# Performance work log

Hardware: AMD Instinct MI355X
Metric: run time of the kernel (lower is better)

## Reference

```python
import jax, jax.numpy as jnp
import numpy as np

TEMPERATURE = 5.656854249492381  # sqrt(d_k)=sqrt(32)


def setup_inputs() -> dict:
    key = jax.random.key(0)
    k1, k2, k3, k4 = jax.random.split(key, 4)
    B, L, H, DK, DV = 4, 1024, 8, 32, 32
    q = jax.random.normal(k1, (B, L, H * DK), dtype=jnp.float32)
    k = jax.random.normal(k2, (B, L, H * DK), dtype=jnp.float32)
    v = jax.random.normal(k3, (B, L, H * DV), dtype=jnp.float32)
    a_k = jax.random.normal(k4, (L, L, DK), dtype=jnp.float32)
    return {"q": q, "k": k, "v": v, "a_k": a_k, "d_k": DK, "d_v": DV, "n_head": H}


def reference(q, k, v, a_k, d_k, d_v, n_head):
    B, Lq, _ = q.shape
    Lv = v.shape[1]
    # [B, H, L, d]
    rq = q.reshape(B, Lq, n_head, d_k).transpose(0, 2, 1, 3)
    rk = k.reshape(B, Lq, n_head, d_k).transpose(0, 2, 1, 3)
    rv = v.reshape(B, Lv, n_head, d_v).transpose(0, 2, 1, 3)
    # attn[b,h,i,j] = sum_d rq[b,h,j,d] * rk[b,h,i,d] * a_k[i,j,d]
    # (dim 2 indexes k positions, dim 3 indexes q positions, per the torch broadcast)
    attn = jnp.einsum('bhjd,bhid,ijd->bhij', rq, rk, a_k) / TEMPERATURE
    attn = jax.nn.softmax(attn, axis=-1)
    # dropout is identity in eval mode
    out = jnp.einsum('bhij,bhjd->bhid', attn, rv)
    return out, attn
```

## Files before the change

kernel.cpp:

```cpp
#include <hip/hip_runtime.h>
#include <cstddef>

#define B_  4
#define L_  1024
#define H_  8
#define DK_ 32
#define DV_ 32
#define BH_ 32
#define HD_ 256

#define INV_T 0.17677669529663687f

__global__ __launch_bounds__(256) void transpose_q(
    const float* __restrict__ q, float* __restrict__ qT)
{
    const int bh  = blockIdx.x >> 2;
    const int jt  = blockIdx.x & 3;
    const int b   = bh >> 3, h = bh & 7;
    const int tid = threadIdx.x;

    __shared__ float t_s[256][33];

    const float* qb = q + (size_t)b * L_ * HD_ + h * DK_;
    #pragma unroll
    for (int rep = 0; rep < 8; ++rep) {
        const int f = rep * 1024 + tid * 4;
        const int j = f >> 5, d = f & 31;
        float4 val = *reinterpret_cast<const float4*>(qb + (size_t)(jt * 256 + j) * HD_ + d);
        t_s[j][d + 0] = val.x; t_s[j][d + 1] = val.y;
        t_s[j][d + 2] = val.z; t_s[j][d + 3] = val.w;
    }
    __syncthreads();
    float* qo = qT + (size_t)bh * (DK_ * L_);
    const int j = jt * 256 + tid;
    #pragma unroll
    for (int d4 = 0; d4 < 8; ++d4) {
        float4 w = make_float4(t_s[tid][d4 * 4 + 0], t_s[tid][d4 * 4 + 1],
                               t_s[tid][d4 * 4 + 2], t_s[tid][d4 * 4 + 3]);
        *reinterpret_cast<float4*>(qo + (size_t)d4 * (L_ * 4) + (size_t)j * 4) = w;
    }
}

__global__ __launch_bounds__(256) void score_kernel(
    const float* __restrict__ qT,
    const float* __restrict__ k,
    const float* __restrict__ a_k,
    float* __restrict__ attn_u,
    float* __restrict__ sums)
{
    const int bidx  = blockIdx.x;
    const int jhalf = bidx & 1;
    const int half  = (bidx >> 1) & 1;
    const int ig    = bidx >> 2;
    const int i0    = ig * 2;
    const int bh0   = half * 16;
    const int tid   = threadIdx.x;
    const int w     = __builtin_amdgcn_readfirstlane(tid >> 6);
    const int lane  = tid & 63;

    __shared__ float a_s[2][64][36];

    float rs[4][2] = {{0.f}};

    for (int jt = jhalf * 8; jt < jhalf * 8 + 8; ++jt) {
        const int j0 = jt * 64;
        __syncthreads();
        #pragma unroll
        for (int rep = 0; rep < 4; ++rep) {
            const int f  = rep * 1024 + tid * 4;
            const int ii = f >> 11, jj = (f >> 5) & 63, d = f & 31;
            float4 val = *reinterpret_cast<const float4*>(
                a_k + (size_t)(i0 + ii) * (L_ * DK_) + (size_t)(j0 + jj) * DK_ + d);
            *reinterpret_cast<float4*>(&a_s[ii][jj][d]) = val;
        }
        __syncthreads();

        float s[4][2];
        #pragma unroll
        for (int bhl = 0; bhl < 4; ++bhl)
            #pragma unroll
            for (int ii = 0; ii < 2; ++ii) s[bhl][ii] = 0.f;

        #pragma unroll 2
        for (int d4 = 0; d4 < 8; ++d4) {
            float4 av[2];
            #pragma unroll
            for (int ii = 0; ii < 2; ++ii)
                av[ii] = *reinterpret_cast<const float4*>(&a_s[ii][lane][d4 * 4]);
            #pragma unroll
            for (int bhl = 0; bhl < 4; ++bhl) {
                const int bh = bh0 + w * 4 + bhl;
                const int b  = bh >> 3, h = bh & 7;
                const float4 q4 = *reinterpret_cast<const float4*>(
                    qT + (size_t)bh * (DK_ * L_) + (size_t)d4 * (L_ * 4) + (size_t)(j0 + lane) * 4);
                const float* kp = k + (size_t)b * L_ * HD_ + (size_t)i0 * HD_ + h * DK_ + d4 * 4;
                #pragma unroll
                for (int ii = 0; ii < 2; ++ii) {
                    float4 kv = *reinterpret_cast<const float4*>(kp + ii * HD_);
                    s[bhl][ii] = fmaf(kv.x * av[ii].x, q4.x, s[bhl][ii]);
                    s[bhl][ii] = fmaf(kv.y * av[ii].y, q4.y, s[bhl][ii]);
                    s[bhl][ii] = fmaf(kv.z * av[ii].z, q4.z, s[bhl][ii]);
                    s[bhl][ii] = fmaf(kv.w * av[ii].w, q4.w, s[bhl][ii]);
                }
            }
        }

        #pragma unroll
        for (int bhl = 0; bhl < 4; ++bhl) {
            const int bh = bh0 + w * 4 + bhl;
            #pragma unroll
            for (int ii = 0; ii < 2; ++ii) {
                const float u = __expf(s[bhl][ii] * INV_T);
                rs[bhl][ii] += u;
                attn_u[((size_t)bh * L_ + (i0 + ii)) * L_ + j0 + lane] = u;
            }
        }
    }

    #pragma unroll
    for (int bhl = 0; bhl < 4; ++bhl) {
        #pragma unroll
        for (int ii = 0; ii < 2; ++ii) {
            float vsum = rs[bhl][ii];
            #pragma unroll
            for (int off = 32; off > 0; off >>= 1) vsum += __shfl_xor(vsum, off);
            if (lane == 0)
                sums[((size_t)jhalf * BH_ + bh0 + w * 4 + bhl) * L_ + i0 + ii] = vsum;
        }
    }
}

__global__ __launch_bounds__(256) void pv_kernel(
    const float* __restrict__ v,
    const float* __restrict__ sums,
    float* __restrict__ attn,
    float* __restrict__ out)
{
    const int bh  = blockIdx.x >> 6;
    const int ic  = blockIdx.x & 63;
    const int i0  = ic * 16;
    const int b   = bh >> 3, h = bh & 7;
    const int tid = threadIdx.x;
    const int r   = tid >> 4;
    const int t16 = tid & 15;

    __shared__ float v_s[64][36];
    __shared__ float u_s[16][68];

    const float inv = 1.0f / (sums[(size_t)bh * L_ + i0 + r] +
                              sums[(size_t)(BH_ + bh) * L_ + i0 + r]);
    float* arow = attn + ((size_t)bh * L_ + i0 + r) * L_;

    float a0 = 0.f, a1 = 0.f;

    for (int jt = 0; jt < 16; ++jt) {
        const int j0 = jt * 64;
        __syncthreads();
        {
            const int jj = tid >> 2, dv = (tid & 3) * 8;
            const float* vp = v + (size_t)b * L_ * HD_ + (size_t)(j0 + jj) * HD_ + h * DV_ + dv;
            float4 v0 = *reinterpret_cast<const float4*>(vp);
            float4 v1 = *reinterpret_cast<const float4*>(vp + 4);
            *reinterpret_cast<float4*>(&v_s[jj][dv])     = v0;
            *reinterpret_cast<float4*>(&v_s[jj][dv + 4]) = v1;
        }
        {
            float4 u0 = *reinterpret_cast<const float4*>(arow + j0 + t16 * 4);
            u0.x *= inv; u0.y *= inv; u0.z *= inv; u0.w *= inv;
            *reinterpret_cast<float4*>(&u_s[r][t16 * 4]) = u0;
            *reinterpret_cast<float4*>(arow + j0 + t16 * 4) = u0;
        }
        __syncthreads();
        #pragma unroll
        for (int jj4 = 0; jj4 < 16; ++jj4) {
            const float4 u4 = *reinterpret_cast<const float4*>(&u_s[r][jj4 * 4]);
            const float2 vv0 = *reinterpret_cast<const float2*>(&v_s[jj4 * 4 + 0][t16 * 2]);
            const float2 vv1 = *reinterpret_cast<const float2*>(&v_s[jj4 * 4 + 1][t16 * 2]);
            const float2 vv2 = *reinterpret_cast<const float2*>(&v_s[jj4 * 4 + 2][t16 * 2]);
            const float2 vv3 = *reinterpret_cast<const float2*>(&v_s[jj4 * 4 + 3][t16 * 2]);
            a0 = fmaf(u4.x, vv0.x, a0); a1 = fmaf(u4.x, vv0.y, a1);
            a0 = fmaf(u4.y, vv1.x, a0); a1 = fmaf(u4.y, vv1.y, a1);
            a0 = fmaf(u4.z, vv2.x, a0); a1 = fmaf(u4.z, vv2.y, a1);
            a0 = fmaf(u4.w, vv3.x, a0); a1 = fmaf(u4.w, vv3.y, a1);
        }
    }
    *reinterpret_cast<float2*>(out + ((size_t)bh * L_ + i0 + r) * DV_ + t16 * 2)
        = make_float2(a0, a1);
}

extern "C" void kernel_launch(void* const* d_in, const int* in_sizes, int n_in,
                              void* d_out, int out_size, void* d_ws, size_t ws_size,
                              hipStream_t stream) {
    const float* q   = (const float*)d_in[0];
    const float* k   = (const float*)d_in[1];
    const float* v   = (const float*)d_in[2];
    const float* a_k = (const float*)d_in[3];

    float* out  = (float*)d_out;
    float* attn = out + (size_t)BH_ * L_ * DV_;

    float* ws   = (float*)d_ws;
    float* sums = ws;
    float* qT   = ws + 2 * BH_ * L_;

    transpose_q<<<dim3(128),   dim3(256), 0, stream>>>(q, qT);
    score_kernel<<<dim3(2048), dim3(256), 0, stream>>>(qT, k, a_k, attn, sums);
    pv_kernel<<<dim3(2048),    dim3(256), 0, stream>>>(v, sums, attn, out);
}
```

Before: 408.4 us.

## Double-buffer score and PV tiles with direct global-to-LDS loads and XOR swizzle

```diff
diff --git a/kernel.cpp b/kernel.cpp
--- a/kernel.cpp
+++ b/kernel.cpp
@@ -1,5 +1,6 @@
 #include <hip/hip_runtime.h>
 #include <cstddef>
+#include <cstdint>
 
 #define B_  4
 #define L_  1024
@@ -10,6 +11,13 @@
 #define HD_ 256
 
 #define INV_T 0.17677669529663687f
+
+__device__ __forceinline__ void gload_lds16(const void* g, void* l) {
+    __builtin_amdgcn_global_load_lds(
+        (const __attribute__((address_space(1))) void*)g,
+        (__attribute__((address_space(3))) void*)l,
+        16, 0, 0);
+}
 
 __global__ __launch_bounds__(256) void transpose_q(
     const float* __restrict__ q, float* __restrict__ qT)
@@ -58,22 +66,40 @@
     const int w     = __builtin_amdgcn_readfirstlane(tid >> 6);
     const int lane  = tid & 63;
 
-    __shared__ float a_s[2][64][36];
+    __shared__ __align__(16) float a_s[2][2][64][32];
+
+    int s_ii[4], s_jj[4], s_c[4];
+    #pragma unroll
+    for (int r2 = 0; r2 < 4; ++r2) {
+        const int off = r2 * 4096 + tid * 16;
+        s_ii[r2] = off >> 13;
+        s_jj[r2] = (off >> 7) & 63;
+        s_c[r2]  = ((off >> 4) & 7) ^ (s_jj[r2] & 7);
+    }
+
+    auto STAGE = [&](int buf, int j0s) {
+        #pragma unroll
+        for (int r2 = 0; r2 < 4; ++r2) {
+            const float* src = a_k + (size_t)(i0 + s_ii[r2]) * (L_ * DK_)
+                             + (size_t)(j0s + s_jj[r2]) * DK_ + s_c[r2] * 4;
+            float* dst = (float*)((char*)(&a_s[buf][0][0][0]) + r2 * 4096 + w * 1024);
+            gload_lds16(src, dst);
+        }
+    };
 
     float rs[4][2] = {{0.f}};
-
-    for (int jt = jhalf * 8; jt < jhalf * 8 + 8; ++jt) {
-        const int j0 = jt * 64;
-        __syncthreads();
-        #pragma unroll
-        for (int rep = 0; rep < 4; ++rep) {
-            const int f  = rep * 1024 + tid * 4;
-            const int ii = f >> 11, jj = (f >> 5) & 63, d = f & 31;
-            float4 val = *reinterpret_cast<const float4*>(
-                a_k + (size_t)(i0 + ii) * (L_ * DK_) + (size_t)(j0 + jj) * DK_ + d);
-            *reinterpret_cast<float4*>(&a_s[ii][jj][d]) = val;
-        }
-        __syncthreads();
+    const int jt0 = jhalf * 8, jtE = jt0 + 8;
+    int cur = 0;
+
+    STAGE(0, jt0 * 64);
+    asm volatile("s_waitcnt vmcnt(0)" ::: "memory");
+    __builtin_amdgcn_s_barrier();
+
+    for (int jt = jt0; jt < jtE; ++jt) {
+        const int j0   = jt * 64;
+        const bool more = (jt != jtE - 1);
+
+        if (more) STAGE(cur ^ 1, j0 + 64);
 
         float s[4][2];
         #pragma unroll
@@ -86,7 +112,9 @@
             float4 av[2];
             #pragma unroll
             for (int ii = 0; ii < 2; ++ii)
-                av[ii] = *reinterpret_cast<const float4*>(&a_s[ii][lane][d4 * 4]);
+                av[ii] = *reinterpret_cast<const float4*>(
+                    (const char*)(&a_s[cur][ii][0][0]) + lane * 128
+                    + ((d4 ^ (lane & 7)) << 4));
             #pragma unroll
             for (int bhl = 0; bhl < 4; ++bhl) {
                 const int bh = bh0 + w * 4 + bhl;
@@ -115,6 +143,12 @@
                 attn_u[((size_t)bh * L_ + (i0 + ii)) * L_ + j0 + lane] = u;
             }
         }
+
+        if (more) {
+            asm volatile("s_waitcnt vmcnt(0)" ::: "memory");
+            __builtin_amdgcn_s_barrier();
+            cur ^= 1;
+        }
     }
 
     #pragma unroll
@@ -141,51 +175,73 @@
     const int i0  = ic * 16;
     const int b   = bh >> 3, h = bh & 7;
     const int tid = threadIdx.x;
+    const int w   = __builtin_amdgcn_readfirstlane(tid >> 6);
     const int r   = tid >> 4;
     const int t16 = tid & 15;
 
-    __shared__ float v_s[64][36];
-    __shared__ float u_s[16][68];
+    __shared__ __align__(16) float v_s[2][64][32];
+    __shared__ __align__(16) float u_s[2][16][64];
 
     const float inv = 1.0f / (sums[(size_t)bh * L_ + i0 + r] +
                               sums[(size_t)(BH_ + bh) * L_ + i0 + r]);
     float* arow = attn + ((size_t)bh * L_ + i0 + r) * L_;
 
+    const int u_c = t16 ^ (r & 3);
+    const float* u_src0 = arow + u_c * 4;
+    const float* vbase = v + (size_t)b * L_ * HD_ + h * DV_;
+    const int v_jj0 = tid >> 3, v_dc = tid & 7;
+
+    auto STAGE = [&](int buf, int j0s) {
+        gload_lds16(u_src0 + j0s, (float*)((char*)(&u_s[buf][0][0]) + w * 1024));
+        #pragma unroll
+        for (int s2 = 0; s2 < 2; ++s2)
+            gload_lds16(vbase + (size_t)(j0s + s2 * 32 + v_jj0) * HD_ + v_dc * 4,
+                        (float*)((char*)(&v_s[buf][0][0]) + s2 * 4096 + w * 1024));
+    };
+
     float a0 = 0.f, a1 = 0.f;
+    int cur = 0;
+
+    STAGE(0, 0);
+    asm volatile("s_waitcnt vmcnt(0)" ::: "memory");
+    __builtin_amdgcn_s_barrier();
 
     for (int jt = 0; jt < 16; ++jt) {
-        const int j0 = jt * 64;
-        __syncthreads();
+        const int j0   = jt * 64;
+        const bool more = (jt != 15);
+
+        if (more) STAGE(cur ^ 1, j0 + 64);
+
         {
-            const int jj = tid >> 2, dv = (tid & 3) * 8;
-            const float* vp = v + (size_t)b * L_ * HD_ + (size_t)(j0 + jj) * HD_ + h * DV_ + dv;
-            float4 v0 = *reinterpret_cast<const float4*>(vp);
-            float4 v1 = *reinterpret_cast<const float4*>(vp + 4);
-            *reinterpret_cast<float4*>(&v_s[jj][dv])     = v0;
-            *reinterpret_cast<float4*>(&v_s[jj][dv + 4]) = v1;
-        }
-        {
-            float4 u0 = *reinterpret_cast<const float4*>(arow + j0 + t16 * 4);
-            u0.x *= inv; u0.y *= inv; u0.z *= inv; u0.w *= inv;
-            *reinterpret_cast<float4*>(&u_s[r][t16 * 4]) = u0;
-            *reinterpret_cast<float4*>(arow + j0 + t16 * 4) = u0;
-        }
-        __syncthreads();
+            const float4 uw = *reinterpret_cast<const float4*>(
+                (const char*)(&u_s[cur][0][0]) + r * 256 + ((t16 ^ (r & 3)) << 4));
+            float4 pw = make_float4(uw.x * inv, uw.y * inv, uw.z * inv, uw.w * inv);
+            *reinterpret_cast<float4*>(arow + j0 + t16 * 4) = pw;
+        }
+
         #pragma unroll
         for (int jj4 = 0; jj4 < 16; ++jj4) {
-            const float4 u4 = *reinterpret_cast<const float4*>(&u_s[r][jj4 * 4]);
-            const float2 vv0 = *reinterpret_cast<const float2*>(&v_s[jj4 * 4 + 0][t16 * 2]);
-            const float2 vv1 = *reinterpret_cast<const float2*>(&v_s[jj4 * 4 + 1][t16 * 2]);
-            const float2 vv2 = *reinterpret_cast<const float2*>(&v_s[jj4 * 4 + 2][t16 * 2]);
-            const float2 vv3 = *reinterpret_cast<const float2*>(&v_s[jj4 * 4 + 3][t16 * 2]);
+            const float4 u4 = *reinterpret_cast<const float4*>(
+                (const char*)(&u_s[cur][0][0]) + r * 256 + ((jj4 ^ (r & 3)) << 4));
+            const float2 vv0 = *reinterpret_cast<const float2*>(&v_s[cur][jj4 * 4 + 0][t16 * 2]);
+            const float2 vv1 = *reinterpret_cast<const float2*>(&v_s[cur][jj4 * 4 + 1][t16 * 2]);
+            const float2 vv2 = *reinterpret_cast<const float2*>(&v_s[cur][jj4 * 4 + 2][t16 * 2]);
+            const float2 vv3 = *reinterpret_cast<const float2*>(&v_s[cur][jj4 * 4 + 3][t16 * 2]);
             a0 = fmaf(u4.x, vv0.x, a0); a1 = fmaf(u4.x, vv0.y, a1);
             a0 = fmaf(u4.y, vv1.x, a0); a1 = fmaf(u4.y, vv1.y, a1);
             a0 = fmaf(u4.z, vv2.x, a0); a1 = fmaf(u4.z, vv2.y, a1);
             a0 = fmaf(u4.w, vv3.x, a0); a1 = fmaf(u4.w, vv3.y, a1);
         }
-    }
+
+        if (more) {
+            asm volatile("s_waitcnt vmcnt(0)" ::: "memory");
+            __builtin_amdgcn_s_barrier();
+            cur ^= 1;
+        }
+    }
+
     *reinterpret_cast<float2*>(out + ((size_t)bh * L_ + i0 + r) * DV_ + t16 * 2)
-        = make_float2(a0, a1);
+        = make_float2(a0 * inv, a1 * inv);
 }
 
 extern "C" void kernel_launch(void* const* d_in, const int* in_sizes, int n_in,
```

Result: slower. 421.2 us (+3.1%).
